# Kernel optimization log

Measured on AMD Instinct MI355X. Metric: run time of the kernel, lower is better.

The kernel has to match this reference:

```python
import jax, jax.numpy as jnp
import numpy as np

B, N, C, H, K = 4, 8192, 512, 8, 256
D = C // H  # head_dim = 64
EPS = 1e-6


def setup_inputs() -> dict:
    key = jax.random.key(0)
    k1, k2, k3 = jax.random.split(key, 3)
    x = jax.random.normal(k1, (B, N, C), dtype=jnp.float32)
    # Dense kernel (Keras default glorot-ish scale approximated; exact init irrelevant for math check)
    w_qkvv = jax.random.normal(k2, (C, 4 * C), dtype=jnp.float32) * (1.0 / np.sqrt(C))
    # UniformSqrtDim: uniform(-1/sqrt(K), 1/sqrt(K)) over shape (N, K)
    lim = 1.0 / np.sqrt(K)
    spatial_proj = jax.random.uniform(k3, (N, K), minval=-lim, maxval=lim, dtype=jnp.float32)
    temp_ca = jnp.ones((H, 1, 1), dtype=jnp.float32)
    temp_sa = jnp.ones((H, 1, 1), dtype=jnp.float32)
    return {"x": x, "w_qkvv": w_qkvv, "spatial_proj": spatial_proj,
            "temp_ca": temp_ca, "temp_sa": temp_sa}


def _safe_normalize(t):
    # normalize along last axis with clamped squared-sum (matches safe_normalize)
    sq = jnp.sum(t * t, axis=-1, keepdims=True)
    sq = jnp.where(sq < EPS, EPS, sq)
    return t / jnp.sqrt(sq)


def reference(x, w_qkvv, spatial_proj, temp_ca, temp_sa):
    b, n, c = x.shape
    qkvv = x @ w_qkvv  # [B, N, 4C]
    qkvv = qkvv.reshape(b, n, 4, H, D).transpose(2, 0, 3, 1, 4)  # [4, B, H, N, D]
    q, k, v_ca, v_sa = qkvv[0], qkvv[1], qkvv[2], qkvv[3]
    # transpose to [B, H, D, N]; normalize along N (tokens)
    q_t = q.transpose(0, 1, 3, 2)
    k_t = k.transpose(0, 1, 3, 2)
    v_ca_t = v_ca.transpose(0, 1, 3, 2)
    v_sa_t = v_sa.transpose(0, 1, 3, 2)
    q_norm = _safe_normalize(q_t)  # [B, H, D, N]
    k_norm = _safe_normalize(k_t)

    # --- Channel attention: [B,H,D,D] over small head_dim ---
    attn_ca = jnp.einsum('bhdn,bhen->bhde', q_norm, k_norm) * temp_ca
    attn_ca = jax.nn.softmax(attn_ca, axis=-1)
    x_ca = jnp.einsum('bhde,bhen->bhdn', attn_ca, v_ca_t)  # [B,H,D,N]
    x_ca = x_ca.transpose(0, 3, 1, 2).reshape(b, n, c)  # [B,N,C]

    # --- Spatial attention with N->K token projection ---
    k_proj = jnp.einsum('bhdn,nk->bhdk', k_norm, spatial_proj)  # [B,H,D,K]
    v_proj = jnp.einsum('bhdn,nk->bhdk', v_sa_t, spatial_proj)  # [B,H,D,K]
    attn_sa = jnp.einsum('bhdn,bhdk->bhnk', q_norm, k_proj) * temp_sa  # [B,H,N,K]
    attn_sa = jax.nn.softmax(attn_sa, axis=-1)
    x_sa = jnp.einsum('bhnk,bhdk->bhnd', attn_sa, v_proj)  # [B,H,N,D]
    x_sa = x_sa.transpose(0, 2, 1, 3).reshape(b, n, c)

    return x_ca + x_sa
```

## Files before the change

kernel.cpp:

```cpp
#include <hip/hip_runtime.h>
#include <hip/hip_bf16.h>

#define BATCH 4
#define SEQ   8192
#define CH    512
#define NHEAD 8
#define HDIM  64
#define KTOK  256
#define FOURC 2048

typedef __attribute__((ext_vector_type(8))) short bf16x8;
typedef __attribute__((ext_vector_type(4))) float f32x4;

#define GLOAD_LDS16(g, l)                                                      \
  __builtin_amdgcn_global_load_lds(                                            \
      (const __attribute__((address_space(1))) void*)(g),                      \
      (__attribute__((address_space(3))) void*)(l), 16, 0, 0)

__device__ __forceinline__ ushort bf16bits(float f) {
  __hip_bfloat16 b = __float2bfloat16(f);
  return *reinterpret_cast<ushort*>(&b);
}
__device__ __forceinline__ uint packbf2(float lo, float hi) {
  return (uint)bf16bits(lo) | ((uint)bf16bits(hi) << 16);
}

__global__ __launch_bounds__(256) void k_wt(
    const float* __restrict__ W, __hip_bfloat16* __restrict__ Wt) {
  __shared__ float tile[32][33];
  const int bx = blockIdx.x * 32;
  const int by = blockIdx.y * 32;
  const int t = threadIdx.x;
  const int r = t >> 5, c = t & 31;
#pragma unroll
  for (int it = 0; it < 4; ++it)
    tile[r + it * 8][c] = W[(size_t)(by + r + it * 8) * FOURC + bx + c];
  __syncthreads();
#pragma unroll
  for (int it = 0; it < 4; ++it) {
    int n = r + it * 8;
    Wt[(size_t)(bx + n) * CH + by + c] = __float2bfloat16(tile[c][n]);
  }
}

__global__ __launch_bounds__(256) void k_pt(
    const float* __restrict__ P, __hip_bfloat16* __restrict__ Pt) {
  __shared__ float tile[32][33];
  const int n0 = blockIdx.x * 32, k0 = blockIdx.y * 32;
  const int t = threadIdx.x, r = t >> 5, c = t & 31;
#pragma unroll
  for (int i = 0; i < 4; ++i)
    tile[r + i * 8][c] = P[(size_t)(n0 + r + i * 8) * KTOK + k0 + c];
  __syncthreads();
#pragma unroll
  for (int i = 0; i < 4; ++i)
    Pt[(size_t)(k0 + r + i * 8) * SEQ + n0 + c] = __float2bfloat16(tile[c][r + i * 8]);
}

__global__ __launch_bounds__(256) void k_xbf(
    const float* __restrict__ X, __hip_bfloat16* __restrict__ Xb) {
  size_t i = ((size_t)blockIdx.x * 256 + threadIdx.x) * 8;
  float4 a = *reinterpret_cast<const float4*>(&X[i]);
  float4 b = *reinterpret_cast<const float4*>(&X[i + 4]);
  ushort tmp[8];
  tmp[0] = bf16bits(a.x); tmp[1] = bf16bits(a.y);
  tmp[2] = bf16bits(a.z); tmp[3] = bf16bits(a.w);
  tmp[4] = bf16bits(b.x); tmp[5] = bf16bits(b.y);
  tmp[6] = bf16bits(b.z); tmp[7] = bf16bits(b.w);
  *reinterpret_cast<uint4*>(&Xb[i]) = *reinterpret_cast<const uint4*>(tmp);
}

__global__ __launch_bounds__(256) void k_gemm_mfma(
    const __hip_bfloat16* __restrict__ Xb, const __hip_bfloat16* __restrict__ Wt,
    __hip_bfloat16* __restrict__ QKVV) {
  __shared__ __align__(16) __hip_bfloat16 As[3][128 * 32];
  __shared__ __align__(16) __hip_bfloat16 Bs[3][128 * 32];
  const int t = threadIdx.x;
  const int wid = t >> 6, lane = t & 63;
  const int bid = blockIdx.x;
  const int xcd = bid & 7;
  const int l = bid >> 3;
  const int bm = (xcd * 32 + (l >> 4)) * 128;
  const int bn = (l & 15) * 128;
  const int wr = wid >> 1, wc = wid & 1;
  const int lrow = lane & 15;
  const int lk = (((lane >> 4) ^ ((lrow >> 1) & 3))) * 8;
  const int srow = lane >> 2;
  const int sk8 = (((lane & 3) ^ ((lane >> 3) & 3))) * 8;
  const int c0 = wid * 2, c1 = wid * 2 + 1;
  f32x4 acc[4][4] = {};

#define STAGE(bufi, kk)                                                         \
  do {                                                                          \
    GLOAD_LDS16(&Xb[(size_t)(bm + c0 * 16 + srow) * CH + (kk) + sk8],           \
                &As[bufi][c0 * 512]);                                           \
    GLOAD_LDS16(&Wt[(size_t)(bn + c0 * 16 + srow) * CH + (kk) + sk8],           \
                &Bs[bufi][c0 * 512]);                                           \
    GLOAD_LDS16(&Xb[(size_t)(bm + c1 * 16 + srow) * CH + (kk) + sk8],           \
                &As[bufi][c1 * 512]);                                           \
    GLOAD_LDS16(&Wt[(size_t)(bn + c1 * 16 + srow) * CH + (kk) + sk8],           \
                &Bs[bufi][c1 * 512]);                                           \
  } while (0)

  STAGE(0, 0);
  STAGE(1, 32);
#pragma unroll
  for (int kt = 0; kt < 16; ++kt) {
    const int cur = kt % 3;
    if (kt < 14) {
      STAGE((kt + 2) % 3, (kt + 2) * 32);
      asm volatile("s_waitcnt vmcnt(8)" ::: "memory");
    } else if (kt == 14) {
      asm volatile("s_waitcnt vmcnt(4)" ::: "memory");
    } else {
      asm volatile("s_waitcnt vmcnt(0)" ::: "memory");
    }
    __builtin_amdgcn_s_barrier();
    bf16x8 af[4], bfr[4];
#pragma unroll
    for (int i = 0; i < 4; ++i)
      af[i] = *reinterpret_cast<const bf16x8*>(&As[cur][(wr * 64 + i * 16 + lrow) * 32 + lk]);
#pragma unroll
    for (int j = 0; j < 4; ++j)
      bfr[j] = *reinterpret_cast<const bf16x8*>(&Bs[cur][(wc * 64 + j * 16 + lrow) * 32 + lk]);
#pragma unroll
    for (int i = 0; i < 4; ++i)
#pragma unroll
      for (int j = 0; j < 4; ++j)
        acc[i][j] = __builtin_amdgcn_mfma_f32_16x16x32_bf16(af[i], bfr[j], acc[i][j], 0, 0, 0);
    asm volatile("s_waitcnt lgkmcnt(0)" ::: "memory");
    __builtin_amdgcn_s_barrier();
  }
#undef STAGE
  const int l4 = (lane >> 4) * 4;
#pragma unroll
  for (int i = 0; i < 4; ++i)
#pragma unroll
    for (int j = 0; j < 4; ++j) {
      int col = bn + wc * 64 + j * 16 + lrow;
#pragma unroll
      for (int r = 0; r < 4; ++r) {
        int row = bm + wr * 64 + i * 16 + l4 + r;
        QKVV[(size_t)row * FOURC + col] = __float2bfloat16(acc[i][j][r]);
      }
    }
}

__global__ __launch_bounds__(256) void k_qkstats(
    const __hip_bfloat16* __restrict__ QKVV,
    const __hip_bfloat16* __restrict__ Pt,
    float* __restrict__ G, float* __restrict__ sumsq, float* __restrict__ raw) {
  __shared__ __hip_bfloat16 qT[64][40];
  __shared__ __hip_bfloat16 kT[64][40];
  __shared__ __hip_bfloat16 vT[64][40];
  __shared__ __hip_bfloat16 pT[256][40];
  __shared__ float red[32][64];
  const int bh = blockIdx.y, b = bh >> 3, h = bh & 7;
  const int nbase = blockIdx.x * 1024;
  const int t = threadIdx.x, w = t >> 6, lane = t & 63;
  const int l15 = lane & 15, g = lane >> 4;
  const int comp = w >> 1, kh = w & 1;
  const int srow = t >> 3, sdq = (t & 7) * 8;
  const int scol = srow ^ ((t & 3) << 3);
  const int prow = t >> 2, poff = (t & 3) * 8;
  int gq[4], gw;
  {
#pragma unroll
    for (int dt = 0; dt < 4; ++dt) gq[dt] = (g ^ (((dt * 16 + l15) >> 3) & 3)) * 8;
    gw = (g ^ (((w * 16 + l15) >> 3) & 3)) * 8;
  }
  f32x4 acc[4][8] = {};
  f32x4 accg[4] = {};
  float sqq[8] = {}, sqk[8] = {};
  uint4 uq, uk, uv, up0, up1, up2, up3;
  {
    size_t gb = (size_t)(b * SEQ + nbase + srow) * FOURC + h * HDIM + sdq;
    uq = *reinterpret_cast<const uint4*>(&QKVV[gb]);
    uk = *reinterpret_cast<const uint4*>(&QKVV[gb + CH]);
    uv = *reinterpret_cast<const uint4*>(&QKVV[gb + 3 * CH]);
    up0 = *reinterpret_cast<const uint4*>(&Pt[(size_t)(0 * 64 + prow) * SEQ + nbase + poff]);
    up1 = *reinterpret_cast<const uint4*>(&Pt[(size_t)(1 * 64 + prow) * SEQ + nbase + poff]);
    up2 = *reinterpret_cast<const uint4*>(&Pt[(size_t)(2 * 64 + prow) * SEQ + nbase + poff]);
    up3 = *reinterpret_cast<const uint4*>(&Pt[(size_t)(3 * 64 + prow) * SEQ + nbase + poff]);
  }
  for (int it = 0; it < 32; ++it) {
    {
      const __hip_bfloat16* hq = reinterpret_cast<const __hip_bfloat16*>(&uq);
      const __hip_bfloat16* hk = reinterpret_cast<const __hip_bfloat16*>(&uk);
      const __hip_bfloat16* hv = reinterpret_cast<const __hip_bfloat16*>(&uv);
#pragma unroll
      for (int j = 0; j < 8; ++j) {
        float fq = __bfloat162float(hq[j]);
        float fk = __bfloat162float(hk[j]);
        sqq[j] = fmaf(fq, fq, sqq[j]);
        sqk[j] = fmaf(fk, fk, sqk[j]);
        qT[sdq + j][scol] = hq[j];
        kT[sdq + j][scol] = hk[j];
        vT[sdq + j][scol] = hv[j];
      }
      *reinterpret_cast<uint4*>(&pT[0 * 64 + prow][poff]) = up0;
      *reinterpret_cast<uint4*>(&pT[1 * 64 + prow][poff]) = up1;
      *reinterpret_cast<uint4*>(&pT[2 * 64 + prow][poff]) = up2;
      *reinterpret_cast<uint4*>(&pT[3 * 64 + prow][poff]) = up3;
    }
    if (it < 31) {
      const int nn = nbase + (it + 1) * 32;
      size_t gb = (size_t)(b * SEQ + nn + srow) * FOURC + h * HDIM + sdq;
      uq = *reinterpret_cast<const uint4*>(&QKVV[gb]);
      uk = *reinterpret_cast<const uint4*>(&QKVV[gb + CH]);
      uv = *reinterpret_cast<const uint4*>(&QKVV[gb + 3 * CH]);
      up0 = *reinterpret_cast<const uint4*>(&Pt[(size_t)(0 * 64 + prow) * SEQ + nn + poff]);
      up1 = *reinterpret_cast<const uint4*>(&Pt[(size_t)(1 * 64 + prow) * SEQ + nn + poff]);
      up2 = *reinterpret_cast<const uint4*>(&Pt[(size_t)(2 * 64 + prow) * SEQ + nn + poff]);
      up3 = *reinterpret_cast<const uint4*>(&Pt[(size_t)(3 * 64 + prow) * SEQ + nn + poff]);
    }
    __syncthreads();
    {
      bf16x8 Aq[4];
#pragma unroll
      for (int dt = 0; dt < 4; ++dt)
        Aq[dt] = *reinterpret_cast<const bf16x8*>(&qT[dt * 16 + l15][gq[dt]]);
      bf16x8 Bk = *reinterpret_cast<const bf16x8*>(&kT[w * 16 + l15][gw]);
#pragma unroll
      for (int dt = 0; dt < 4; ++dt)
        accg[dt] = __builtin_amdgcn_mfma_f32_16x16x32_bf16(Aq[dt], Bk, accg[dt], 0, 0, 0);
    }
    {
      bf16x8 A[4], B[8];
#pragma unroll
      for (int dt = 0; dt < 4; ++dt)
        A[dt] = comp ? *reinterpret_cast<const bf16x8*>(&vT[dt * 16 + l15][gq[dt]])
                     : *reinterpret_cast<const bf16x8*>(&kT[dt * 16 + l15][gq[dt]]);
#pragma unroll
      for (int kt = 0; kt < 8; ++kt)
        B[kt] = *reinterpret_cast<const bf16x8*>(&pT[(kh * 8 + kt) * 16 + l15][g * 8]);
#pragma unroll
      for (int dt = 0; dt < 4; ++dt)
#pragma unroll
        for (int kt = 0; kt < 8; ++kt)
          acc[dt][kt] = __builtin_amdgcn_mfma_f32_16x16x32_bf16(A[dt], B[kt], acc[dt][kt], 0, 0, 0);
    }
    __syncthreads();
  }
#pragma unroll
  for (int j = 0; j < 8; ++j) red[srow][sdq + j] = sqq[j];
  __syncthreads();
  if (t < 64) {
    float tot = 0.f;
#pragma unroll
    for (int r = 0; r < 32; ++r) tot += red[r][t];
    atomicAdd(&sumsq[bh * 64 + t], tot);
  }
  __syncthreads();
#pragma unroll
  for (int j = 0; j < 8; ++j) red[srow][sdq + j] = sqk[j];
  __syncthreads();
  if (t < 64) {
    float tot = 0.f;
#pragma unroll
    for (int r = 0; r < 32; ++r) tot += red[r][t];
    atomicAdd(&sumsq[2048 + bh * 64 + t], tot);
  }
  float* gp = G + (size_t)bh * 4096;
#pragma unroll
  for (int dt = 0; dt < 4; ++dt)
#pragma unroll
    for (int r = 0; r < 4; ++r)
      atomicAdd(&gp[(dt * 16 + g * 4 + r) * 64 + w * 16 + l15], accg[dt][r]);
  float* rp = raw + ((size_t)bh * 2 + comp) * (64 * 256);
#pragma unroll
  for (int dt = 0; dt < 4; ++dt)
#pragma unroll
    for (int kt = 0; kt < 8; ++kt)
#pragma unroll
      for (int r = 0; r < 4; ++r)
        atomicAdd(&rp[(dt * 16 + g * 4 + r) * 256 + (kh * 8 + kt) * 16 + l15],
                  acc[dt][kt][r]);
}

__global__ __launch_bounds__(256) void k_epi(
    const float* __restrict__ sumsq, const float* __restrict__ G,
    const float* __restrict__ raw, const float* __restrict__ tca,
    const float* __restrict__ tsa, __hip_bfloat16* __restrict__ Gb,
    __hip_bfloat16* __restrict__ kpT, __hip_bfloat16* __restrict__ vpT) {
  __shared__ float iqs[64], iks[64];
  __shared__ float tile[64][65];
  const int bh = blockIdx.x, h = bh & 7;
  const int t = threadIdx.x;
  if (t < 64) {
    iqs[t] = rsqrtf(fmaxf(sumsq[bh * 64 + t], 1e-6f));
    iks[t] = rsqrtf(fmaxf(sumsq[2048 + bh * 64 + t], 1e-6f));
  }
  __syncthreads();
  if (t < 64) {
    const float* row = G + (size_t)bh * 4096 + t * 64;
    const float s0 = iqs[t] * tca[h];
    float vals[64];
    float m = -3.0e38f;
#pragma unroll
    for (int e = 0; e < 64; ++e) {
      float v = row[e] * s0 * iks[e];
      vals[e] = v;
      m = fmaxf(m, v);
    }
    float s = 0.f;
#pragma unroll
    for (int e = 0; e < 64; ++e) { vals[e] = __expf(vals[e] - m); s += vals[e]; }
    float r = 1.0f / s;
#pragma unroll
    for (int e = 0; e < 64; ++e)
      Gb[(size_t)bh * 4096 + t * 64 + e] = __float2bfloat16(vals[e] * r);
  }
  const float ts = tsa[h];
  const float* r0 = raw + (size_t)bh * 2 * 16384;
  for (int kc = 0; kc < 4; ++kc) {
    __syncthreads();
    for (int i = t; i < 4096; i += 256) {
      int d = i >> 6, kk = i & 63;
      tile[d][kk] = r0[d * 256 + kc * 64 + kk];
    }
    __syncthreads();
    for (int i = t; i < 4096; i += 256) {
      int kk = i >> 6, d = i & 63;
      float sc = iqs[d] * iks[d] * ts;
      kpT[(size_t)bh * 16384 + (kc * 64 + kk) * 64 + d] = __float2bfloat16(tile[d][kk] * sc);
    }
  }
  const float* r1 = r0 + 16384;
  for (int i = t; i < 16384; i += 256)
    vpT[(size_t)bh * 16384 + i] = __float2bfloat16(r1[i]);
}

__global__ __launch_bounds__(256) void k_xout(
    const __hip_bfloat16* __restrict__ QKVV,
    const __hip_bfloat16* __restrict__ Gb,
    const __hip_bfloat16* __restrict__ kpT,
    const __hip_bfloat16* __restrict__ vpT,
    float* __restrict__ out) {
  __shared__ __hip_bfloat16 vs[64][264];
  __shared__ __hip_bfloat16 ps[4][16][264];
  __shared__ __hip_bfloat16 gs[64][72];
  const int bh = blockIdx.y, b = bh >> 3, h = bh & 7;
  const int nblk = blockIdx.x * 512;
  const int t = threadIdx.x, w = t >> 6, lane = t & 63;
  const int l15 = lane & 15, g = lane >> 4;
  for (int i = t; i < 2048; i += 256) {
    int d = i >> 5, k8 = (i & 31) * 8;
    *reinterpret_cast<uint4*>(&vs[d][k8]) =
        *reinterpret_cast<const uint4*>(&vpT[((size_t)bh * 64 + d) * 256 + k8]);
  }
  for (int i = t; i < 512; i += 256) {
    int row = i >> 3, q = i & 7;
    *reinterpret_cast<uint4*>(&gs[row][q * 8]) =
        *reinterpret_cast<const uint4*>(&Gb[(size_t)bh * 4096 + row * 64 + q * 8]);
  }
  bf16x8 kA[2][16];
#pragma unroll
  for (int s = 0; s < 2; ++s)
#pragma unroll
    for (int f = 0; f < 16; ++f)
      kA[s][f] = *reinterpret_cast<const bf16x8*>(
          &kpT[((size_t)bh * 256 + f * 16 + l15) * 64 + s * 32 + g * 8]);
  __syncthreads();
  const __hip_bfloat16* qbase = QKVV + (size_t)b * SEQ * FOURC + h * HDIM;
  const __hip_bfloat16* vbase = qbase + 2 * CH;
  bf16x8 qf[2], vf[2];
#pragma unroll
  for (int s = 0; s < 2; ++s) {
    qf[s] = *reinterpret_cast<const bf16x8*>(
        &qbase[(size_t)(nblk + w * 16 + l15) * FOURC + s * 32 + g * 8]);
    vf[s] = *reinterpret_cast<const bf16x8*>(
        &vbase[(size_t)(nblk + w * 16 + l15) * FOURC + s * 32 + g * 8]);
  }
  for (int c = w; c < 32; c += 4) {
    const int n0 = nblk + c * 16;
    bf16x8 qn[2], vn[2];
    if (c + 4 < 32) {
#pragma unroll
      for (int s = 0; s < 2; ++s) {
        qn[s] = *reinterpret_cast<const bf16x8*>(
            &qbase[(size_t)(n0 + 64 + l15) * FOURC + s * 32 + g * 8]);
        vn[s] = *reinterpret_cast<const bf16x8*>(
            &vbase[(size_t)(n0 + 64 + l15) * FOURC + s * 32 + g * 8]);
      }
    }
    f32x4 o[4] = {};
#pragma unroll
    for (int dt = 0; dt < 4; ++dt) {
      bf16x8 g0 = *reinterpret_cast<const bf16x8*>(&gs[dt * 16 + l15][g * 8]);
      bf16x8 g1 = *reinterpret_cast<const bf16x8*>(&gs[dt * 16 + l15][32 + g * 8]);
      o[dt] = __builtin_amdgcn_mfma_f32_16x16x32_bf16(vf[0], g0, o[dt], 0, 0, 0);
      o[dt] = __builtin_amdgcn_mfma_f32_16x16x32_bf16(vf[1], g1, o[dt], 0, 0, 0);
    }
    f32x4 acc[16] = {};
#pragma unroll
    for (int f = 0; f < 16; ++f) {
      acc[f] = __builtin_amdgcn_mfma_f32_16x16x32_bf16(kA[0][f], qf[0], acc[f], 0, 0, 0);
      acc[f] = __builtin_amdgcn_mfma_f32_16x16x32_bf16(kA[1][f], qf[1], acc[f], 0, 0, 0);
    }
    float m = -3.0e38f;
#pragma unroll
    for (int f = 0; f < 16; ++f)
#pragma unroll
      for (int r = 0; r < 4; ++r) m = fmaxf(m, acc[f][r]);
    m = fmaxf(m, __shfl_xor(m, 16));
    m = fmaxf(m, __shfl_xor(m, 32));
    float sum = 0.f;
#pragma unroll
    for (int f = 0; f < 16; ++f)
#pragma unroll
      for (int r = 0; r < 4; ++r) {
        float e = __expf(acc[f][r] - m);
        acc[f][r] = e; sum += e;
      }
    sum += __shfl_xor(sum, 16);
    sum += __shfl_xor(sum, 32);
    const float rinv = 1.0f / sum;
#pragma unroll
    for (int f = 0; f < 16; ++f) {
      uint2 pw;
      pw.x = packbf2(acc[f][0] * rinv, acc[f][1] * rinv);
      pw.y = packbf2(acc[f][2] * rinv, acc[f][3] * rinv);
      *reinterpret_cast<uint2*>(&ps[w][l15][f * 16 + g * 4]) = pw;
    }
    __builtin_amdgcn_wave_barrier();
#pragma unroll
    for (int s = 0; s < 8; ++s) {
      bf16x8 pa = *reinterpret_cast<const bf16x8*>(&ps[w][l15][s * 32 + g * 8]);
#pragma unroll
      for (int dt = 0; dt < 4; ++dt) {
        bf16x8 vb = *reinterpret_cast<const bf16x8*>(&vs[dt * 16 + l15][s * 32 + g * 8]);
        o[dt] = __builtin_amdgcn_mfma_f32_16x16x32_bf16(pa, vb, o[dt], 0, 0, 0);
      }
    }
#pragma unroll
    for (int dt = 0; dt < 4; ++dt)
#pragma unroll
      for (int r = 0; r < 4; ++r) {
        size_t oo = ((size_t)(b * SEQ + n0 + g * 4 + r)) * CH + h * HDIM + dt * 16 + l15;
        out[oo] = o[dt][r];
      }
    qf[0] = qn[0]; qf[1] = qn[1];
    vf[0] = vn[0]; vf[1] = vn[1];
    __builtin_amdgcn_wave_barrier();
  }
}

extern "C" void kernel_launch(void* const* d_in, const int* in_sizes, int n_in,
                              void* d_out, int out_size, void* d_ws, size_t ws_size,
                              hipStream_t stream) {
  const float* x   = (const float*)d_in[0];
  const float* w   = (const float*)d_in[1];
  const float* sp  = (const float*)d_in[2];
  const float* tca = (const float*)d_in[3];
  const float* tsa = (const float*)d_in[4];
  float* out = (float*)d_out;
  char* ws = (char*)d_ws;

  __hip_bfloat16* qkvv = (__hip_bfloat16*)ws;
  __hip_bfloat16* wt   = (__hip_bfloat16*)(ws + 134217728);
  __hip_bfloat16* pt   = (__hip_bfloat16*)(ws + 136314880);
  __hip_bfloat16* xb   = (__hip_bfloat16*)(ws + 140509184);
  __hip_bfloat16* gb   = (__hip_bfloat16*)(ws + 140509184);
  __hip_bfloat16* kpT  = (__hip_bfloat16*)(ws + 174063616);
  __hip_bfloat16* vpT  = (__hip_bfloat16*)(ws + 175112192);
  float* G     = (float*)(ws + 176177152);
  float* sumsq = (float*)(ws + 176701440);
  float* raw   = (float*)(ws + 176717824);

  hipMemsetAsync(G, 0, 524288 + 16384 + 4194304, stream);

  hipLaunchKernelGGL(k_wt, dim3(64, 16), dim3(256), 0, stream, w, wt);
  hipLaunchKernelGGL(k_pt, dim3(256, 8), dim3(256), 0, stream, sp, pt);
  hipLaunchKernelGGL(k_xbf, dim3(8192), dim3(256), 0, stream, x, xb);
  hipLaunchKernelGGL(k_gemm_mfma, dim3(4096), dim3(256), 0, stream, xb, wt, qkvv);
  hipLaunchKernelGGL(k_qkstats, dim3(8, 32), dim3(256), 0, stream, qkvv, pt, G, sumsq, raw);
  hipLaunchKernelGGL(k_epi, dim3(32), dim3(256), 0, stream, sumsq, G, raw, tca, tsa,
                     gb, kpT, vpT);
  hipLaunchKernelGGL(k_xout, dim3(16, 32), dim3(256), 0, stream, qkvv, gb, kpT, vpT, out);
}
```

Before: 266.9 us.

## Split GEMM output into Q/Vca row-major and transposed K/Vsa, fuse sumsq into GEMM

The QKV GEMM epilogue now writes Q and V_ca to a narrower row-major buffer and K and V_sa in a token-contiguous transposed layout. It also accumulates the per-channel squared norms of Q and K via LDS and global atomics. The stats kernel can then stage K, V and P tiles straight into LDS with async global-to-LDS loads in a double buffer, dropping its register transpose and sum-of-squares reduction. The costs are scattered transposed stores in the GEMM epilogue and extra atomics there.

Result: slower. 295.7 us (+10.8%).

```diff
diff --git a/kernel.cpp b/kernel.cpp
--- a/kernel.cpp
+++ b/kernel.cpp
@@ -8,6 +8,7 @@
 #define HDIM  64
 #define KTOK  256
 #define FOURC 2048
+#define V2C   1024
 
 typedef __attribute__((ext_vector_type(8))) short bf16x8;
 typedef __attribute__((ext_vector_type(4))) float f32x4;
@@ -72,9 +73,11 @@
 
 __global__ __launch_bounds__(256) void k_gemm_mfma(
     const __hip_bfloat16* __restrict__ Xb, const __hip_bfloat16* __restrict__ Wt,
-    __hip_bfloat16* __restrict__ QKVV) {
+    __hip_bfloat16* __restrict__ QKVV2, __hip_bfloat16* __restrict__ QKVT,
+    float* __restrict__ sumsq) {
   __shared__ __align__(16) __hip_bfloat16 As[3][128 * 32];
   __shared__ __align__(16) __hip_bfloat16 Bs[3][128 * 32];
+  __shared__ float csum[128];
   const int t = threadIdx.x;
   const int wid = t >> 6, lane = t & 63;
   const int bid = blockIdx.x;
@@ -88,6 +91,7 @@
   const int srow = lane >> 2;
   const int sk8 = (((lane & 3) ^ ((lane >> 3) & 3))) * 8;
   const int c0 = wid * 2, c1 = wid * 2 + 1;
+  if (t < 128) csum[t] = 0.f;
   f32x4 acc[4][4] = {};
 
 #define STAGE(bufi, kk)                                                         \
@@ -133,28 +137,66 @@
   }
 #undef STAGE
   const int l4 = (lane >> 4) * 4;
-#pragma unroll
-  for (int i = 0; i < 4; ++i)
+  const int comp = bn >> 9;
+  const int b = bm >> 13;
+  if (comp == 0 || comp == 2) {
+    const int cbase = (comp == 0) ? 0 : 512;
+#pragma unroll
+    for (int i = 0; i < 4; ++i)
+#pragma unroll
+      for (int j = 0; j < 4; ++j) {
+        int col2 = cbase + (bn & 511) + wc * 64 + j * 16 + lrow;
+#pragma unroll
+        for (int r = 0; r < 4; ++r) {
+          int row = bm + wr * 64 + i * 16 + l4 + r;
+          QKVV2[(size_t)row * V2C + col2] = __float2bfloat16(acc[i][j][r]);
+        }
+      }
+  } else {
+    const int cp = (comp == 1) ? 0 : 1;
+#pragma unroll
+    for (int i = 0; i < 4; ++i)
+#pragma unroll
+      for (int j = 0; j < 4; ++j) {
+        int colg = bn + wc * 64 + j * 16 + lrow;
+        int h = (colg >> 6) & 7, d = colg & 63;
+        int nb = (bm & 8191) + wr * 64 + i * 16 + l4;
+        ushort4 tmp;
+        tmp.x = bf16bits(acc[i][j][0]); tmp.y = bf16bits(acc[i][j][1]);
+        tmp.z = bf16bits(acc[i][j][2]); tmp.w = bf16bits(acc[i][j][3]);
+        *reinterpret_cast<ushort4*>(
+            &QKVT[(((size_t)((cp * 32 + b * 8 + h) * 64 + d)) << 13) + nb]) = tmp;
+      }
+  }
+  if (comp == 0 || comp == 1) {
 #pragma unroll
     for (int j = 0; j < 4; ++j) {
-      int col = bn + wc * 64 + j * 16 + lrow;
-#pragma unroll
-      for (int r = 0; r < 4; ++r) {
-        int row = bm + wr * 64 + i * 16 + l4 + r;
-        QKVV[(size_t)row * FOURC + col] = __float2bfloat16(acc[i][j][r]);
-      }
-    }
+      int coll = wc * 64 + j * 16 + lrow;
+      float s = 0.f;
+#pragma unroll
+      for (int i = 0; i < 4; ++i)
+#pragma unroll
+        for (int r = 0; r < 4; ++r) s = fmaf(acc[i][j][r], acc[i][j][r], s);
+      atomicAdd(&csum[coll], s);
+    }
+    __syncthreads();
+    if (t < 128) {
+      int colg = bn + t;
+      int h = (colg >> 6) & 7, d = colg & 63;
+      atomicAdd(&sumsq[(comp == 0 ? 0 : 2048) + (b * 8 + h) * 64 + d], csum[t]);
+    }
+  }
 }
 
 __global__ __launch_bounds__(256) void k_qkstats(
-    const __hip_bfloat16* __restrict__ QKVV,
+    const __hip_bfloat16* __restrict__ QKVV2,
+    const __hip_bfloat16* __restrict__ QKVT,
     const __hip_bfloat16* __restrict__ Pt,
-    float* __restrict__ G, float* __restrict__ sumsq, float* __restrict__ raw) {
+    float* __restrict__ G, float* __restrict__ raw) {
   __shared__ __hip_bfloat16 qT[64][40];
-  __shared__ __hip_bfloat16 kT[64][40];
-  __shared__ __hip_bfloat16 vT[64][40];
-  __shared__ __hip_bfloat16 pT[256][40];
-  __shared__ float red[32][64];
+  __shared__ __align__(16) __hip_bfloat16 kT2[2][256 * 8];
+  __shared__ __align__(16) __hip_bfloat16 vT2[2][256 * 8];
+  __shared__ __align__(16) __hip_bfloat16 pT2[2][1024 * 8];
   const int bh = blockIdx.y, b = bh >> 3, h = bh & 7;
   const int nbase = blockIdx.x * 1024;
   const int t = threadIdx.x, w = t >> 6, lane = t & 63;
@@ -162,57 +204,47 @@
   const int comp = w >> 1, kh = w & 1;
   const int srow = t >> 3, sdq = (t & 7) * 8;
   const int scol = srow ^ ((t & 3) << 3);
-  const int prow = t >> 2, poff = (t & 3) * 8;
-  int gq[4], gw;
-  {
-#pragma unroll
-    for (int dt = 0; dt < 4; ++dt) gq[dt] = (g ^ (((dt * 16 + l15) >> 3) & 3)) * 8;
-    gw = (g ^ (((w * 16 + l15) >> 3) & 3)) * 8;
-  }
+  int gq[4];
+#pragma unroll
+  for (int dt = 0; dt < 4; ++dt) gq[dt] = (g ^ (((dt * 16 + l15) >> 3) & 3)) * 8;
+  const __hip_bfloat16* kbase = QKVT + ((size_t)(0 * 32 + bh) * 64) * SEQ;
+  const __hip_bfloat16* vbase = QKVT + ((size_t)(1 * 32 + bh) * 64) * SEQ;
   f32x4 acc[4][8] = {};
   f32x4 accg[4] = {};
-  float sqq[8] = {}, sqk[8] = {};
-  uint4 uq, uk, uv, up0, up1, up2, up3;
-  {
-    size_t gb = (size_t)(b * SEQ + nbase + srow) * FOURC + h * HDIM + sdq;
-    uq = *reinterpret_cast<const uint4*>(&QKVV[gb]);
-    uk = *reinterpret_cast<const uint4*>(&QKVV[gb + CH]);
-    uv = *reinterpret_cast<const uint4*>(&QKVV[gb + 3 * CH]);
-    up0 = *reinterpret_cast<const uint4*>(&Pt[(size_t)(0 * 64 + prow) * SEQ + nbase + poff]);
-    up1 = *reinterpret_cast<const uint4*>(&Pt[(size_t)(1 * 64 + prow) * SEQ + nbase + poff]);
-    up2 = *reinterpret_cast<const uint4*>(&Pt[(size_t)(2 * 64 + prow) * SEQ + nbase + poff]);
-    up3 = *reinterpret_cast<const uint4*>(&Pt[(size_t)(3 * 64 + prow) * SEQ + nbase + poff]);
-  }
+  uint4 uq;
+
+#define STAGE_G(bi, n0)                                                         \
+  do {                                                                          \
+    GLOAD_LDS16(&kbase[(size_t)lane * SEQ + (n0) + w * 8], &kT2[bi][(w * 64) * 8]); \
+    GLOAD_LDS16(&vbase[(size_t)lane * SEQ + (n0) + w * 8], &vT2[bi][(w * 64) * 8]); \
+    GLOAD_LDS16(&Pt[(size_t)(0 * 64 + lane) * SEQ + (n0) + w * 8],              \
+                &pT2[bi][(w * 256 + 0 * 64) * 8]);                              \
+    GLOAD_LDS16(&Pt[(size_t)(1 * 64 + lane) * SEQ + (n0) + w * 8],              \
+                &pT2[bi][(w * 256 + 1 * 64) * 8]);                              \
+    GLOAD_LDS16(&Pt[(size_t)(2 * 64 + lane) * SEQ + (n0) + w * 8],              \
+                &pT2[bi][(w * 256 + 2 * 64) * 8]);                              \
+    GLOAD_LDS16(&Pt[(size_t)(3 * 64 + lane) * SEQ + (n0) + w * 8],              \
+                &pT2[bi][(w * 256 + 3 * 64) * 8]);                              \
+  } while (0)
+
+  STAGE_G(0, nbase);
+  uq = *reinterpret_cast<const uint4*>(
+      &QKVV2[(size_t)(b * SEQ + nbase + srow) * V2C + h * HDIM + sdq]);
   for (int it = 0; it < 32; ++it) {
+    const int cur = it & 1;
+    if (it < 31) STAGE_G(cur ^ 1, nbase + (it + 1) * 32);
     {
       const __hip_bfloat16* hq = reinterpret_cast<const __hip_bfloat16*>(&uq);
-      const __hip_bfloat16* hk = reinterpret_cast<const __hip_bfloat16*>(&uk);
-      const __hip_bfloat16* hv = reinterpret_cast<const __hip_bfloat16*>(&uv);
-#pragma unroll
-      for (int j = 0; j < 8; ++j) {
-        float fq = __bfloat162float(hq[j]);
-        float fk = __bfloat162float(hk[j]);
-        sqq[j] = fmaf(fq, fq, sqq[j]);
-        sqk[j] = fmaf(fk, fk, sqk[j]);
-        qT[sdq + j][scol] = hq[j];
-        kT[sdq + j][scol] = hk[j];
-        vT[sdq + j][scol] = hv[j];
-      }
-      *reinterpret_cast<uint4*>(&pT[0 * 64 + prow][poff]) = up0;
-      *reinterpret_cast<uint4*>(&pT[1 * 64 + prow][poff]) = up1;
-      *reinterpret_cast<uint4*>(&pT[2 * 64 + prow][poff]) = up2;
-      *reinterpret_cast<uint4*>(&pT[3 * 64 + prow][poff]) = up3;
-    }
+#pragma unroll
+      for (int j = 0; j < 8; ++j) qT[sdq + j][scol] = hq[j];
+    }
+    if (it < 31)
+      uq = *reinterpret_cast<const uint4*>(
+          &QKVV2[(size_t)(b * SEQ + nbase + (it + 1) * 32 + srow) * V2C + h * HDIM + sdq]);
     if (it < 31) {
-      const int nn = nbase + (it + 1) * 32;
-      size_t gb = (size_t)(b * SEQ + nn + srow) * FOURC + h * HDIM + sdq;
-      uq = *reinterpret_cast<const uint4*>(&QKVV[gb]);
-      uk = *reinterpret_cast<const uint4*>(&QKVV[gb + CH]);
-      uv = *reinterpret_cast<const uint4*>(&QKVV[gb + 3 * CH]);
-      up0 = *reinterpret_cast<const uint4*>(&Pt[(size_t)(0 * 64 + prow) * SEQ + nn + poff]);
-      up1 = *reinterpret_cast<const uint4*>(&Pt[(size_t)(1 * 64 + prow) * SEQ + nn + poff]);
-      up2 = *reinterpret_cast<const uint4*>(&Pt[(size_t)(2 * 64 + prow) * SEQ + nn + poff]);
-      up3 = *reinterpret_cast<const uint4*>(&Pt[(size_t)(3 * 64 + prow) * SEQ + nn + poff]);
+      asm volatile("s_waitcnt vmcnt(7)" ::: "memory");
+    } else {
+      asm volatile("s_waitcnt vmcnt(0)" ::: "memory");
     }
     __syncthreads();
     {
@@ -220,7 +252,7 @@
 #pragma unroll
       for (int dt = 0; dt < 4; ++dt)
         Aq[dt] = *reinterpret_cast<const bf16x8*>(&qT[dt * 16 + l15][gq[dt]]);
-      bf16x8 Bk = *reinterpret_cast<const bf16x8*>(&kT[w * 16 + l15][gw]);
+      bf16x8 Bk = *reinterpret_cast<const bf16x8*>(&kT2[cur][(g * 64 + w * 16 + l15) * 8]);
 #pragma unroll
       for (int dt = 0; dt < 4; ++dt)
         accg[dt] = __builtin_amdgcn_mfma_f32_16x16x32_bf16(Aq[dt], Bk, accg[dt], 0, 0, 0);
@@ -229,11 +261,13 @@
       bf16x8 A[4], B[8];
 #pragma unroll
       for (int dt = 0; dt < 4; ++dt)
-        A[dt] = comp ? *reinterpret_cast<const bf16x8*>(&vT[dt * 16 + l15][gq[dt]])
-                     : *reinterpret_cast<const bf16x8*>(&kT[dt * 16 + l15][gq[dt]]);
+        A[dt] = comp
+            ? *reinterpret_cast<const bf16x8*>(&vT2[cur][(g * 64 + dt * 16 + l15) * 8])
+            : *reinterpret_cast<const bf16x8*>(&kT2[cur][(g * 64 + dt * 16 + l15) * 8]);
 #pragma unroll
       for (int kt = 0; kt < 8; ++kt)
-        B[kt] = *reinterpret_cast<const bf16x8*>(&pT[(kh * 8 + kt) * 16 + l15][g * 8]);
+        B[kt] = *reinterpret_cast<const bf16x8*>(
+            &pT2[cur][(g * 256 + (kh * 8 + kt) * 16 + l15) * 8]);
 #pragma unroll
       for (int dt = 0; dt < 4; ++dt)
 #pragma unroll
@@ -242,25 +276,7 @@
     }
     __syncthreads();
   }
-#pragma unroll
-  for (int j = 0; j < 8; ++j) red[srow][sdq + j] = sqq[j];
-  __syncthreads();
-  if (t < 64) {
-    float tot = 0.f;
-#pragma unroll
-    for (int r = 0; r < 32; ++r) tot += red[r][t];
-    atomicAdd(&sumsq[bh * 64 + t], tot);
-  }
-  __syncthreads();
-#pragma unroll
-  for (int j = 0; j < 8; ++j) red[srow][sdq + j] = sqk[j];
-  __syncthreads();
-  if (t < 64) {
-    float tot = 0.f;
-#pragma unroll
-    for (int r = 0; r < 32; ++r) tot += red[r][t];
-    atomicAdd(&sumsq[2048 + bh * 64 + t], tot);
-  }
+#undef STAGE_G
   float* gp = G + (size_t)bh * 4096;
 #pragma unroll
   for (int dt = 0; dt < 4; ++dt)
@@ -332,7 +348,7 @@
 }
 
 __global__ __launch_bounds__(256) void k_xout(
-    const __hip_bfloat16* __restrict__ QKVV,
+    const __hip_bfloat16* __restrict__ QKVV2,
     const __hip_bfloat16* __restrict__ Gb,
     const __hip_bfloat16* __restrict__ kpT,
     const __hip_bfloat16* __restrict__ vpT,
@@ -362,15 +378,15 @@
       kA[s][f] = *reinterpret_cast<const bf16x8*>(
           &kpT[((size_t)bh * 256 + f * 16 + l15) * 64 + s * 32 + g * 8]);
   __syncthreads();
-  const __hip_bfloat16* qbase = QKVV + (size_t)b * SEQ * FOURC + h * HDIM;
-  const __hip_bfloat16* vbase = qbase + 2 * CH;
+  const __hip_bfloat16* qbase = QKVV2 + (size_t)b * SEQ * V2C + h * HDIM;
+  const __hip_bfloat16* vbase = qbase + 512;
   bf16x8 qf[2], vf[2];
 #pragma unroll
   for (int s = 0; s < 2; ++s) {
     qf[s] = *reinterpret_cast<const bf16x8*>(
-        &qbase[(size_t)(nblk + w * 16 + l15) * FOURC + s * 32 + g * 8]);
+        &qbase[(size_t)(nblk + w * 16 + l15) * V2C + s * 32 + g * 8]);
     vf[s] = *reinterpret_cast<const bf16x8*>(
-        &vbase[(size_t)(nblk + w * 16 + l15) * FOURC + s * 32 + g * 8]);
+        &vbase[(size_t)(nblk + w * 16 + l15) * V2C + s * 32 + g * 8]);
   }
   for (int c = w; c < 32; c += 4) {
     const int n0 = nblk + c * 16;
@@ -379,9 +395,9 @@
 #pragma unroll
       for (int s = 0; s < 2; ++s) {
         qn[s] = *reinterpret_cast<const bf16x8*>(
-            &qbase[(size_t)(n0 + 64 + l15) * FOURC + s * 32 + g * 8]);
+            &qbase[(size_t)(n0 + 64 + l15) * V2C + s * 32 + g * 8]);
         vn[s] = *reinterpret_cast<const bf16x8*>(
-            &vbase[(size_t)(n0 + 64 + l15) * FOURC + s * 32 + g * 8]);
+            &vbase[(size_t)(n0 + 64 + l15) * V2C + s * 32 + g * 8]);
       }
     }
     f32x4 o[4] = {};
@@ -457,13 +473,14 @@
   float* out = (float*)d_out;
   char* ws = (char*)d_ws;
 
-  __hip_bfloat16* qkvv = (__hip_bfloat16*)ws;
-  __hip_bfloat16* wt   = (__hip_bfloat16*)(ws + 134217728);
-  __hip_bfloat16* pt   = (__hip_bfloat16*)(ws + 136314880);
-  __hip_bfloat16* xb   = (__hip_bfloat16*)(ws + 140509184);
-  __hip_bfloat16* gb   = (__hip_bfloat16*)(ws + 140509184);
-  __hip_bfloat16* kpT  = (__hip_bfloat16*)(ws + 174063616);
-  __hip_bfloat16* vpT  = (__hip_bfloat16*)(ws + 175112192);
+  __hip_bfloat16* qkvv2 = (__hip_bfloat16*)ws;
+  __hip_bfloat16* qkvt  = (__hip_bfloat16*)(ws + 67108864);
+  __hip_bfloat16* wt    = (__hip_bfloat16*)(ws + 134217728);
+  __hip_bfloat16* pt    = (__hip_bfloat16*)(ws + 136314880);
+  __hip_bfloat16* xb    = (__hip_bfloat16*)(ws + 140509184);
+  __hip_bfloat16* gb    = (__hip_bfloat16*)(ws + 140509184);
+  __hip_bfloat16* kpT   = (__hip_bfloat16*)(ws + 174063616);
+  __hip_bfloat16* vpT   = (__hip_bfloat16*)(ws + 175112192);
   float* G     = (float*)(ws + 176177152);
   float* sumsq = (float*)(ws + 176701440);
   float* raw   = (float*)(ws + 176717824);
@@ -473,9 +490,10 @@
   hipLaunchKernelGGL(k_wt, dim3(64, 16), dim3(256), 0, stream, w, wt);
   hipLaunchKernelGGL(k_pt, dim3(256, 8), dim3(256), 0, stream, sp, pt);
   hipLaunchKernelGGL(k_xbf, dim3(8192), dim3(256), 0, stream, x, xb);
-  hipLaunchKernelGGL(k_gemm_mfma, dim3(4096), dim3(256), 0, stream, xb, wt, qkvv);
-  hipLaunchKernelGGL(k_qkstats, dim3(8, 32), dim3(256), 0, stream, qkvv, pt, G, sumsq, raw);
+  hipLaunchKernelGGL(k_gemm_mfma, dim3(4096), dim3(256), 0, stream, xb, wt,
+                     qkvv2, qkvt, sumsq);
+  hipLaunchKernelGGL(k_qkstats, dim3(8, 32), dim3(256), 0, stream, qkvv2, qkvt, pt, G, raw);
   hipLaunchKernelGGL(k_epi, dim3(32), dim3(256), 0, stream, sumsq, G, raw, tca, tsa,
                      gb, kpT, vpT);
-  hipLaunchKernelGGL(k_xout, dim3(16, 32), dim3(256), 0, stream, qkvv, gb, kpT, vpT, out);
-}
+  hipLaunchKernelGGL(k_xout, dim3(16, 32), dim3(256), 0, stream, qkvv2, gb, kpT, vpT, out);
+}
```

## Fuse prep kernels and memset into one launch, split qkstats over more blocks

Applied to the files above, without the earlier changes.

Merges the weight transpose, projection transpose, x-to-bf16 conversion and the workspace zeroing memset into a single k_prep kernel. Block-index ranges pick which of the four jobs each block does, which removes three launches plus a memset call. Separately, k_qkstats now covers 512 tokens per block instead of 1024 and its grid doubles to 16x32, so more CUs are busy. The cost is twice as many partial reductions accumulated into G/raw.

After: 289.1 us. 8.3% more time.

```diff
diff --git a/kernel.cpp b/kernel.cpp
--- a/kernel.cpp
+++ b/kernel.cpp
@@ -25,49 +25,54 @@
   return (uint)bf16bits(lo) | ((uint)bf16bits(hi) << 16);
 }
 
-__global__ __launch_bounds__(256) void k_wt(
-    const float* __restrict__ W, __hip_bfloat16* __restrict__ Wt) {
-  __shared__ float tile[32][33];
-  const int bx = blockIdx.x * 32;
-  const int by = blockIdx.y * 32;
+__global__ __launch_bounds__(256) void k_prep(
+    const float* __restrict__ W, const float* __restrict__ P,
+    const float* __restrict__ X, __hip_bfloat16* __restrict__ Wt,
+    __hip_bfloat16* __restrict__ Pt, __hip_bfloat16* __restrict__ Xb,
+    float* __restrict__ Z) {
+  const int bid = blockIdx.x;
   const int t = threadIdx.x;
-  const int r = t >> 5, c = t & 31;
-#pragma unroll
-  for (int it = 0; it < 4; ++it)
-    tile[r + it * 8][c] = W[(size_t)(by + r + it * 8) * FOURC + bx + c];
-  __syncthreads();
-#pragma unroll
-  for (int it = 0; it < 4; ++it) {
-    int n = r + it * 8;
-    Wt[(size_t)(bx + n) * CH + by + c] = __float2bfloat16(tile[c][n]);
-  }
-}
-
-__global__ __launch_bounds__(256) void k_pt(
-    const float* __restrict__ P, __hip_bfloat16* __restrict__ Pt) {
-  __shared__ float tile[32][33];
-  const int n0 = blockIdx.x * 32, k0 = blockIdx.y * 32;
-  const int t = threadIdx.x, r = t >> 5, c = t & 31;
-#pragma unroll
-  for (int i = 0; i < 4; ++i)
-    tile[r + i * 8][c] = P[(size_t)(n0 + r + i * 8) * KTOK + k0 + c];
-  __syncthreads();
-#pragma unroll
-  for (int i = 0; i < 4; ++i)
-    Pt[(size_t)(k0 + r + i * 8) * SEQ + n0 + c] = __float2bfloat16(tile[c][r + i * 8]);
-}
-
-__global__ __launch_bounds__(256) void k_xbf(
-    const float* __restrict__ X, __hip_bfloat16* __restrict__ Xb) {
-  size_t i = ((size_t)blockIdx.x * 256 + threadIdx.x) * 8;
-  float4 a = *reinterpret_cast<const float4*>(&X[i]);
-  float4 b = *reinterpret_cast<const float4*>(&X[i + 4]);
-  ushort tmp[8];
-  tmp[0] = bf16bits(a.x); tmp[1] = bf16bits(a.y);
-  tmp[2] = bf16bits(a.z); tmp[3] = bf16bits(a.w);
-  tmp[4] = bf16bits(b.x); tmp[5] = bf16bits(b.y);
-  tmp[6] = bf16bits(b.z); tmp[7] = bf16bits(b.w);
-  *reinterpret_cast<uint4*>(&Xb[i]) = *reinterpret_cast<const uint4*>(tmp);
+  if (bid < 1024) {
+    __shared__ float tile[32][33];
+    const int bx = (bid & 63) * 32;
+    const int by = (bid >> 6) * 32;
+    const int r = t >> 5, c = t & 31;
+#pragma unroll
+    for (int it = 0; it < 4; ++it)
+      tile[r + it * 8][c] = W[(size_t)(by + r + it * 8) * FOURC + bx + c];
+    __syncthreads();
+#pragma unroll
+    for (int it = 0; it < 4; ++it) {
+      int n = r + it * 8;
+      Wt[(size_t)(bx + n) * CH + by + c] = __float2bfloat16(tile[c][n]);
+    }
+  } else if (bid < 3072) {
+    __shared__ float tile[32][33];
+    const int local = bid - 1024;
+    const int n0 = (local & 255) * 32, k0 = (local >> 8) * 32;
+    const int r = t >> 5, c = t & 31;
+#pragma unroll
+    for (int i = 0; i < 4; ++i)
+      tile[r + i * 8][c] = P[(size_t)(n0 + r + i * 8) * KTOK + k0 + c];
+    __syncthreads();
+#pragma unroll
+    for (int i = 0; i < 4; ++i)
+      Pt[(size_t)(k0 + r + i * 8) * SEQ + n0 + c] = __float2bfloat16(tile[c][r + i * 8]);
+  } else if (bid < 11264) {
+    size_t i = ((size_t)(bid - 3072) * 256 + t) * 8;
+    float4 a = *reinterpret_cast<const float4*>(&X[i]);
+    float4 b = *reinterpret_cast<const float4*>(&X[i + 4]);
+    ushort tmp[8];
+    tmp[0] = bf16bits(a.x); tmp[1] = bf16bits(a.y);
+    tmp[2] = bf16bits(a.z); tmp[3] = bf16bits(a.w);
+    tmp[4] = bf16bits(b.x); tmp[5] = bf16bits(b.y);
+    tmp[6] = bf16bits(b.z); tmp[7] = bf16bits(b.w);
+    *reinterpret_cast<uint4*>(&Xb[i]) = *reinterpret_cast<const uint4*>(tmp);
+  } else {
+    size_t i = (size_t)(bid - 11264) * 256 + t;
+    float4 z = {0.f, 0.f, 0.f, 0.f};
+    *reinterpret_cast<float4*>(reinterpret_cast<char*>(Z) + i * 16) = z;
+  }
 }
 
 __global__ __launch_bounds__(256) void k_gemm_mfma(
@@ -156,7 +161,7 @@
   __shared__ __hip_bfloat16 pT[256][40];
   __shared__ float red[32][64];
   const int bh = blockIdx.y, b = bh >> 3, h = bh & 7;
-  const int nbase = blockIdx.x * 1024;
+  const int nbase = blockIdx.x * 512;
   const int t = threadIdx.x, w = t >> 6, lane = t & 63;
   const int l15 = lane & 15, g = lane >> 4;
   const int comp = w >> 1, kh = w & 1;
@@ -183,7 +188,7 @@
     up2 = *reinterpret_cast<const uint4*>(&Pt[(size_t)(2 * 64 + prow) * SEQ + nbase + poff]);
     up3 = *reinterpret_cast<const uint4*>(&Pt[(size_t)(3 * 64 + prow) * SEQ + nbase + poff]);
   }
-  for (int it = 0; it < 32; ++it) {
+  for (int it = 0; it < 16; ++it) {
     {
       const __hip_bfloat16* hq = reinterpret_cast<const __hip_bfloat16*>(&uq);
       const __hip_bfloat16* hk = reinterpret_cast<const __hip_bfloat16*>(&uk);
@@ -203,7 +208,7 @@
       *reinterpret_cast<uint4*>(&pT[2 * 64 + prow][poff]) = up2;
       *reinterpret_cast<uint4*>(&pT[3 * 64 + prow][poff]) = up3;
     }
-    if (it < 31) {
+    if (it < 15) {
       const int nn = nbase + (it + 1) * 32;
       size_t gb = (size_t)(b * SEQ + nn + srow) * FOURC + h * HDIM + sdq;
       uq = *reinterpret_cast<const uint4*>(&QKVV[gb]);
@@ -468,13 +473,9 @@
   float* sumsq = (float*)(ws + 176701440);
   float* raw   = (float*)(ws + 176717824);
 
-  hipMemsetAsync(G, 0, 524288 + 16384 + 4194304, stream);
-
-  hipLaunchKernelGGL(k_wt, dim3(64, 16), dim3(256), 0, stream, w, wt);
-  hipLaunchKernelGGL(k_pt, dim3(256, 8), dim3(256), 0, stream, sp, pt);
-  hipLaunchKernelGGL(k_xbf, dim3(8192), dim3(256), 0, stream, x, xb);
+  hipLaunchKernelGGL(k_prep, dim3(12420), dim3(256), 0, stream, w, sp, x, wt, pt, xb, G);
   hipLaunchKernelGGL(k_gemm_mfma, dim3(4096), dim3(256), 0, stream, xb, wt, qkvv);
-  hipLaunchKernelGGL(k_qkstats, dim3(8, 32), dim3(256), 0, stream, qkvv, pt, G, sumsq, raw);
+  hipLaunchKernelGGL(k_qkstats, dim3(16, 32), dim3(256), 0, stream, qkvv, pt, G, sumsq, raw);
   hipLaunchKernelGGL(k_epi, dim3(32), dim3(256), 0, stream, sumsq, G, raw, tca, tsa,
                      gb, kpT, vpT);
   hipLaunchKernelGGL(k_xout, dim3(16, 32), dim3(256), 0, stream, qkvv, gb, kpT, vpT, out);
```
